# Kernel optimization log

Hardware: AMD Instinct MI355X
Metric: run time of the kernel (lower is better)

The kernel has to match this reference:

```python
import jax, jax.numpy as jnp
import numpy as np

# EventPropLinear constants (match init_kwargs)
DT = 1.0
TAU_M = 10.0
TAU_S = 1.0
AM = 1.0 - DT / TAU_M   # membrane decay
BM = DT / TAU_M         # membrane input coupling
AS = 1.0 - DT / TAU_S   # synaptic decay


def setup_inputs() -> dict:
    key = jax.random.key(0)
    k1, k2 = jax.random.split(key)
    T, B, IN, OUT = 128, 64, 1024, 1024
    x = jax.random.uniform(k1, (T, B, IN), dtype=jnp.float32)  # input drive / spikes in [0,1)
    # torch.nn.init.normal_(weight, mu, mu) with mu=0.1 -> mean 0.1, std 0.1
    weight = 0.1 + 0.1 * jax.random.normal(k2, (OUT, IN), dtype=jnp.float32)
    return {"x": x, "weight": weight}


def _forward_core(x, weight):
    # x: [T, B, IN]; weight: [OUT, IN]
    T, B, _ = x.shape
    O = weight.shape[0]
    # step i (1..T-1) uses input[i-1]; precompute the linear drive once
    cur = jnp.einsum('tbi,oi->tbo', x[:-1], weight)  # [T-1, B, OUT]

    def step(carry, c):
        V, I = carry
        Vn = AM * V + BM * I
        In = AS * I + c
        s = (Vn > 1.0).astype(x.dtype)
        Vn = (1.0 - s) * Vn           # reset on spike
        return (Vn, In), (s, In)

    z = jnp.zeros((B, O), x.dtype)
    _, (spk, Iseq) = jax.lax.scan(step, (z, z), cur)
    zrow = jnp.zeros((1, B, O), x.dtype)
    out = jnp.concatenate([zrow, spk], axis=0)      # output[0] = 0
    I_full = jnp.concatenate([zrow, Iseq], axis=0)  # I[0] = 0
    return out, I_full


def reference(x, weight):
    # returns spike train [T, B, OUT], matching torch output permuted back to time-major
    return _forward_core(x, weight)[0]
```

## Files before the change

kernel.cpp:

```cpp
#include <hip/hip_runtime.h>
#include <hip/hip_fp8.h>

typedef __attribute__((ext_vector_type(8))) short short8;
typedef __attribute__((ext_vector_type(4))) float f32x4;

__device__ __forceinline__ unsigned short f2bf(float f) {
    unsigned u = __float_as_uint(f);
    u += 0x7FFFu + ((u >> 16) & 1u);
    return (unsigned short)(u >> 16);
}

__device__ __forceinline__ unsigned char f2fp8(float f) {
    __hip_fp8_e4m3 q(f);
    return q.__x;
}

__global__ void eventprop_cvt8_kernel(const float* __restrict__ x, const float* __restrict__ w,
                                      unsigned char* __restrict__ x8, unsigned char* __restrict__ w8,
                                      const int nx, const int ntot)
{
    const int i = blockIdx.x * blockDim.x + threadIdx.x;
    const int e0 = i * 8;
    if (e0 >= ntot) return;
    const float* src;
    unsigned char* dst;
    if (e0 < nx) { src = x + e0; dst = x8 + e0; }
    else         { src = w + (e0 - nx); dst = w8 + (e0 - nx); }
    const float4 f0 = *(const float4*)(src);
    const float4 f1 = *(const float4*)(src + 4);
    uchar4 a, b;
    a.x = f2fp8(f0.x); a.y = f2fp8(f0.y); a.z = f2fp8(f0.z); a.w = f2fp8(f0.w);
    b.x = f2fp8(f1.x); b.y = f2fp8(f1.y); b.z = f2fp8(f1.z); b.w = f2fp8(f1.w);
    uint2 v;
    v.x = *(unsigned int*)&a;
    v.y = *(unsigned int*)&b;
    *(uint2*)dst = v;
}

__global__ __launch_bounds__(256, 4) void eventprop_gemm_fp8_kernel(
    const unsigned char* __restrict__ X8, const unsigned char* __restrict__ W8,
    unsigned short* __restrict__ Cb, const int K, const int N, const int nbn)
{
    __shared__ unsigned char As[128 * 128];
    __shared__ unsigned char Bs[64 * 128];

    const int bid0 = blockIdx.x;
    const int cpx = gridDim.x >> 3;
    const int bid = (bid0 & 7) * cpx + (bid0 >> 3);
    const int bm = bid / nbn, bn = bid % nbn;
    const int m0 = bm * 128, n0 = bn * 64;

    const int tid = threadIdx.x;
    const int lane = tid & 63;
    const int wave = tid >> 6;
    const int wr = wave >> 1, wc = wave & 1;
    const int lrow = lane & 15, kg = lane >> 4;
    const int srow = lane >> 3;
    const int scol = (((lane & 7) ^ srow) * 16);

    f32x4 acc[4][2] = {};

    for (int kt = 0; kt < K; kt += 128) {
        #pragma unroll
        for (int jj = 0; jj < 4; ++jj) {
            const int j = wave * 4 + jj;
            const int row = j * 8 + srow;
            const unsigned char* ga = &X8[(size_t)(m0 + row) * K + kt + scol];
            __builtin_amdgcn_global_load_lds(
                (const __attribute__((address_space(1))) unsigned int*)ga,
                (__attribute__((address_space(3))) unsigned int*)&As[j * 1024], 16, 0, 0);
        }
        #pragma unroll
        for (int jj = 0; jj < 2; ++jj) {
            const int j = wave * 2 + jj;
            const int row = j * 8 + srow;
            const unsigned char* gb = &W8[(size_t)(n0 + row) * K + kt + scol];
            __builtin_amdgcn_global_load_lds(
                (const __attribute__((address_space(1))) unsigned int*)gb,
                (__attribute__((address_space(3))) unsigned int*)&Bs[j * 1024], 16, 0, 0);
        }
        __syncthreads();

        const int rx = (lrow & 7) << 4;
        long a[4][4], b[4][2];
        #pragma unroll
        for (int ks = 0; ks < 4; ++ks) {
            const int cc = (ks * 32 + kg * 8) ^ rx;
            #pragma unroll
            for (int mi = 0; mi < 4; ++mi)
                a[ks][mi] = *(const long*)&As[(wr * 64 + mi * 16 + lrow) * 128 + cc];
            #pragma unroll
            for (int ni = 0; ni < 2; ++ni)
                b[ks][ni] = *(const long*)&Bs[(wc * 32 + ni * 16 + lrow) * 128 + cc];
        }
        #pragma unroll
        for (int ks = 0; ks < 4; ++ks)
            #pragma unroll
            for (int mi = 0; mi < 4; ++mi)
                #pragma unroll
                for (int ni = 0; ni < 2; ++ni)
                    acc[mi][ni] = __builtin_amdgcn_mfma_f32_16x16x32_fp8_fp8(
                        a[ks][mi], b[ks][ni], acc[mi][ni], 0, 0, 0);
        __syncthreads();
    }

    const int r0 = kg * 4;
    #pragma unroll
    for (int mi = 0; mi < 4; ++mi) {
        #pragma unroll
        for (int ni = 0; ni < 2; ++ni) {
            #pragma unroll
            for (int r = 0; r < 4; ++r) {
                const int row = m0 + wr * 64 + mi * 16 + r0 + r;
                const int col = n0 + wc * 32 + ni * 16 + lrow;
                Cb[(size_t)row * N + col] = f2bf(acc[mi][ni][r]);
            }
        }
    }
}

__global__ void eventprop_scan_bf16_kernel(const unsigned short* __restrict__ cur,
                                           float* __restrict__ out, const int BO)
{
    const int j = blockIdx.x * blockDim.x + threadIdx.x;
    const int col = j * 2;
    float V0 = 0.f, I0 = 0.f, V1 = 0.f, I1 = 0.f;
    unsigned int c[8];
    #pragma unroll
    for (int p = 0; p < 8; ++p)
        c[p] = *(const unsigned int*)&cur[(size_t)p * BO + col];
    *(float2*)&out[col] = make_float2(0.f, 0.f);

    #pragma unroll 1
    for (int i = 0; i < 120; i += 8) {
        #pragma unroll
        for (int p = 0; p < 8; ++p) {
            const int it = i + p;
            const unsigned int cn = *(const unsigned int*)&cur[(size_t)(it + 8) * BO + col];
            const float Vn0 = 0.9f * V0 + 0.1f * I0;
            const float Vn1 = 0.9f * V1 + 0.1f * I1;
            const float s0 = (Vn0 > 1.0f) ? 1.0f : 0.0f;
            const float s1 = (Vn1 > 1.0f) ? 1.0f : 0.0f;
            I0 = __uint_as_float(c[p] << 16);
            I1 = __uint_as_float(c[p] & 0xFFFF0000u);
            V0 = (1.0f - s0) * Vn0;
            V1 = (1.0f - s1) * Vn1;
            *(float2*)&out[(size_t)(it + 1) * BO + col] = make_float2(s0, s1);
            c[p] = cn;
        }
    }
    #pragma unroll
    for (int p = 0; p < 7; ++p) {
        const int it = 120 + p;
        const float Vn0 = 0.9f * V0 + 0.1f * I0;
        const float Vn1 = 0.9f * V1 + 0.1f * I1;
        const float s0 = (Vn0 > 1.0f) ? 1.0f : 0.0f;
        const float s1 = (Vn1 > 1.0f) ? 1.0f : 0.0f;
        I0 = __uint_as_float(c[p] << 16);
        I1 = __uint_as_float(c[p] & 0xFFFF0000u);
        V0 = (1.0f - s0) * Vn0;
        V1 = (1.0f - s1) * Vn1;
        *(float2*)&out[(size_t)(it + 1) * BO + col] = make_float2(s0, s1);
    }
}

__global__ __launch_bounds__(256, 2) void eventprop_gemm_f32in_kernel(
    const float* __restrict__ X, const float* __restrict__ W, float* __restrict__ C,
    const int K, const int N, const int nbn)
{
    __shared__ unsigned short As[128][32];
    __shared__ unsigned short Bs[128][32];
    const int bid = blockIdx.x;
    const int bm = bid / nbn, bn = bid % nbn;
    const int m0 = bm * 128, n0 = bn * 128;
    const int tid = threadIdx.x;
    const int lane = tid & 63;
    const int wave = tid >> 6;
    const int wr = wave >> 1, wc = wave & 1;
    const int lrow = lane & 15, kg = lane >> 4;

    f32x4 acc[4][4] = {};
    for (int kt = 0; kt < K; kt += 32) {
        #pragma unroll
        for (int p = 0; p < 4; ++p) {
            const int idx = p * 256 + tid;
            const int row = idx >> 3;
            const int c4  = (idx & 7) * 4;
            const float4 fa = *(const float4*)&X[(size_t)(m0 + row) * K + kt + c4];
            ushort4 ua; ua.x = f2bf(fa.x); ua.y = f2bf(fa.y); ua.z = f2bf(fa.z); ua.w = f2bf(fa.w);
            *(ushort4*)&As[row][c4] = ua;
            const float4 fb = *(const float4*)&W[(size_t)(n0 + row) * K + kt + c4];
            ushort4 ub; ub.x = f2bf(fb.x); ub.y = f2bf(fb.y); ub.z = f2bf(fb.z); ub.w = f2bf(fb.w);
            *(ushort4*)&Bs[row][c4] = ub;
        }
        __syncthreads();
        short8 a[4], b[4];
        #pragma unroll
        for (int mi = 0; mi < 4; ++mi) a[mi] = *(const short8*)&As[wr * 64 + mi * 16 + lrow][kg * 8];
        #pragma unroll
        for (int ni = 0; ni < 4; ++ni) b[ni] = *(const short8*)&Bs[wc * 64 + ni * 16 + lrow][kg * 8];
        #pragma unroll
        for (int mi = 0; mi < 4; ++mi)
            #pragma unroll
            for (int ni = 0; ni < 4; ++ni)
                acc[mi][ni] = __builtin_amdgcn_mfma_f32_16x16x32_bf16(a[mi], b[ni], acc[mi][ni], 0, 0, 0);
        __syncthreads();
    }
    const int r0 = kg * 4;
    #pragma unroll
    for (int mi = 0; mi < 4; ++mi)
        #pragma unroll
        for (int ni = 0; ni < 4; ++ni)
            #pragma unroll
            for (int r = 0; r < 4; ++r)
                C[(size_t)(m0 + wr * 64 + mi * 16 + r0 + r) * N + (n0 + wc * 64 + ni * 16 + lrow)] = acc[mi][ni][r];
}

__global__ void eventprop_scan_kernel(float* __restrict__ out, const int BO)
{
    const int idx = blockIdx.x * blockDim.x + threadIdx.x;
    float V = 0.f, I = 0.f;
    float c[8];
    #pragma unroll
    for (int p = 0; p < 8; ++p)
        c[p] = out[(size_t)p * BO + idx];
    out[idx] = 0.f;
    #pragma unroll 1
    for (int i = 0; i < 120; i += 8) {
        #pragma unroll
        for (int p = 0; p < 8; ++p) {
            const int it = i + p;
            const float cn = out[(size_t)(it + 8) * BO + idx];
            const float Vn = 0.9f * V + 0.1f * I;
            const float s = (Vn > 1.0f) ? 1.0f : 0.0f;
            I = c[p];
            V = (1.0f - s) * Vn;
            out[(size_t)(it + 1) * BO + idx] = s;
            c[p] = cn;
        }
    }
    #pragma unroll
    for (int p = 0; p < 7; ++p) {
        const int it = 120 + p;
        const float Vn = 0.9f * V + 0.1f * I;
        const float s = (Vn > 1.0f) ? 1.0f : 0.0f;
        I = c[p];
        V = (1.0f - s) * Vn;
        out[(size_t)(it + 1) * BO + idx] = s;
    }
}

extern "C" void kernel_launch(void* const* d_in, const int* in_sizes, int n_in,
                              void* d_out, int out_size, void* d_ws, size_t ws_size,
                              hipStream_t stream) {
    const float* x = (const float*)d_in[0];
    const float* w = (const float*)d_in[1];
    float* out = (float*)d_out;

    const int T = 128, B = 64, IN = 1024, OUT = 1024;
    const int Mpad = T * B;
    const int BO = B * OUT;
    const size_t nx = (size_t)Mpad * IN;
    const size_t nw = (size_t)OUT * IN;
    const size_t ncur = (size_t)Mpad * OUT;
    const size_t need = ncur * 2 + nx + nw;

    if (ws_size >= need) {
        unsigned short* curb = (unsigned short*)d_ws;
        unsigned char* x8 = (unsigned char*)(curb + ncur);
        unsigned char* w8 = x8 + nx;
        const int ntot = (int)(nx + nw);
        const int cvt_blocks = (ntot / 8 + 255) / 256;
        eventprop_cvt8_kernel<<<dim3(cvt_blocks), dim3(256), 0, stream>>>(x, w, x8, w8, (int)nx, ntot);
        const int nbn = OUT / 64;
        const int nblocks = (Mpad / 128) * nbn;
        eventprop_gemm_fp8_kernel<<<dim3(nblocks), dim3(256), 0, stream>>>(x8, w8, curb, IN, OUT, nbn);
        eventprop_scan_bf16_kernel<<<dim3((BO / 2) / 256), dim3(256), 0, stream>>>(curb, out, BO);
    } else {
        const int nbn = OUT / 128;
        const int nblocks = (Mpad / 128) * nbn;
        eventprop_gemm_f32in_kernel<<<dim3(nblocks), dim3(256), 0, stream>>>(x, w, out, IN, OUT, nbn);
        eventprop_scan_kernel<<<dim3(BO / 256), dim3(256), 0, stream>>>(out, BO);
    }
}
```

Before: 41.21 us.

## Double-buffer fp8 GEMM LDS tiles with async prefetch two stages ahead

Converts the fp8 GEMM main loop to a double-buffered LDS pipeline: two K-tiles are issued up front, and each iteration waits only on the older tile's loads (vmcnt) before prefetching tile t+2 into the freed buffer while the MFMAs run. The aim is to hide global-to-LDS load latency behind compute instead of serializing load, sync and compute. LDS use doubles to 48KB per block, so launch bounds drop to 3 blocks/CU and occupancy may fall.

```diff
diff --git a/kernel.cpp b/kernel.cpp
--- a/kernel.cpp
+++ b/kernel.cpp
@@ -37,12 +37,12 @@
     *(uint2*)dst = v;
 }
 
-__global__ __launch_bounds__(256, 4) void eventprop_gemm_fp8_kernel(
+__global__ __launch_bounds__(256, 3) void eventprop_gemm_fp8_pipe_kernel(
     const unsigned char* __restrict__ X8, const unsigned char* __restrict__ W8,
     unsigned short* __restrict__ Cb, const int K, const int N, const int nbn)
 {
-    __shared__ unsigned char As[128 * 128];
-    __shared__ unsigned char Bs[64 * 128];
+    __shared__ unsigned char As[2][128 * 128];
+    __shared__ unsigned char Bs[2][64 * 128];
 
     const int bid0 = blockIdx.x;
     const int cpx = gridDim.x >> 3;
@@ -58,9 +58,7 @@
     const int srow = lane >> 3;
     const int scol = (((lane & 7) ^ srow) * 16);
 
-    f32x4 acc[4][2] = {};
-
-    for (int kt = 0; kt < K; kt += 128) {
+    auto stage = [&](int buf, int kt) {
         #pragma unroll
         for (int jj = 0; jj < 4; ++jj) {
             const int j = wave * 4 + jj;
@@ -68,7 +66,7 @@
             const unsigned char* ga = &X8[(size_t)(m0 + row) * K + kt + scol];
             __builtin_amdgcn_global_load_lds(
                 (const __attribute__((address_space(1))) unsigned int*)ga,
-                (__attribute__((address_space(3))) unsigned int*)&As[j * 1024], 16, 0, 0);
+                (__attribute__((address_space(3))) unsigned int*)&As[buf][j * 1024], 16, 0, 0);
         }
         #pragma unroll
         for (int jj = 0; jj < 2; ++jj) {
@@ -77,22 +75,41 @@
             const unsigned char* gb = &W8[(size_t)(n0 + row) * K + kt + scol];
             __builtin_amdgcn_global_load_lds(
                 (const __attribute__((address_space(1))) unsigned int*)gb,
-                (__attribute__((address_space(3))) unsigned int*)&Bs[j * 1024], 16, 0, 0);
-        }
-        __syncthreads();
-
-        const int rx = (lrow & 7) << 4;
+                (__attribute__((address_space(3))) unsigned int*)&Bs[buf][j * 1024], 16, 0, 0);
+        }
+    };
+
+    f32x4 acc[4][2] = {};
+    const int NT = K >> 7;
+    stage(0, 0);
+    stage(1, 128);
+
+    const int rx = (lrow & 7) << 4;
+
+    for (int t = 0; t < NT; ++t) {
+        const int cur = t & 1;
+        if (t + 1 < NT) asm volatile("s_waitcnt vmcnt(6)" ::: "memory");
+        else            asm volatile("s_waitcnt vmcnt(0)" ::: "memory");
+        __builtin_amdgcn_s_barrier();
+        __builtin_amdgcn_sched_barrier(0);
+
         long a[4][4], b[4][2];
         #pragma unroll
         for (int ks = 0; ks < 4; ++ks) {
             const int cc = (ks * 32 + kg * 8) ^ rx;
             #pragma unroll
             for (int mi = 0; mi < 4; ++mi)
-                a[ks][mi] = *(const long*)&As[(wr * 64 + mi * 16 + lrow) * 128 + cc];
+                a[ks][mi] = *(const long*)&As[cur][(wr * 64 + mi * 16 + lrow) * 128 + cc];
             #pragma unroll
             for (int ni = 0; ni < 2; ++ni)
-                b[ks][ni] = *(const long*)&Bs[(wc * 32 + ni * 16 + lrow) * 128 + cc];
-        }
+                b[ks][ni] = *(const long*)&Bs[cur][(wc * 32 + ni * 16 + lrow) * 128 + cc];
+        }
+        asm volatile("s_waitcnt lgkmcnt(0)" ::: "memory");
+        __builtin_amdgcn_sched_barrier(0);
+        __builtin_amdgcn_s_barrier();
+
+        if (t + 2 < NT) stage(cur, (t + 2) << 7);
+
         #pragma unroll
         for (int ks = 0; ks < 4; ++ks)
             #pragma unroll
@@ -101,7 +118,6 @@
                 for (int ni = 0; ni < 2; ++ni)
                     acc[mi][ni] = __builtin_amdgcn_mfma_f32_16x16x32_fp8_fp8(
                         a[ks][mi], b[ks][ni], acc[mi][ni], 0, 0, 0);
-        __syncthreads();
     }
 
     const int r0 = kg * 4;
@@ -274,7 +290,7 @@
         eventprop_cvt8_kernel<<<dim3(cvt_blocks), dim3(256), 0, stream>>>(x, w, x8, w8, (int)nx, ntot);
         const int nbn = OUT / 64;
         const int nblocks = (Mpad / 128) * nbn;
-        eventprop_gemm_fp8_kernel<<<dim3(nblocks), dim3(256), 0, stream>>>(x8, w8, curb, IN, OUT, nbn);
+        eventprop_gemm_fp8_pipe_kernel<<<dim3(nblocks), dim3(256), 0, stream>>>(x8, w8, curb, IN, OUT, nbn);
         eventprop_scan_bf16_kernel<<<dim3((BO / 2) / 256), dim3(256), 0, stream>>>(curb, out, BO);
     } else {
         const int nbn = OUT / 128;
```

Measured after the change: 43.97 us. 6.7% more time.

## Fuse FP8 GEMM with LIF scan by tiling over time per batch row

Applied to the files above, without the earlier changes.

The GEMM is retiled so each block computes all 128 timesteps for one batch index and 64 output columns. The fp32 currents are written to LDS, reusing the A/B staging buffer, and one wave then runs the recurrent scan and writes spikes directly. This removes the bf16 intermediate round-trip through global memory and one kernel launch. In exchange only 64 of 256 threads do the serial scan tail, global A-row reads become strided by batch, and currents stay fp32 instead of being rounded to bf16.

```diff
diff --git a/kernel.cpp b/kernel.cpp
--- a/kernel.cpp
+++ b/kernel.cpp
@@ -37,18 +37,20 @@
     *(uint2*)dst = v;
 }
 
-__global__ __launch_bounds__(256, 4) void eventprop_gemm_fp8_kernel(
+__global__ __launch_bounds__(256, 4) void eventprop_gemm_scan_fp8_kernel(
     const unsigned char* __restrict__ X8, const unsigned char* __restrict__ W8,
-    unsigned short* __restrict__ Cb, const int K, const int N, const int nbn)
-{
-    __shared__ unsigned char As[128 * 128];
-    __shared__ unsigned char Bs[64 * 128];
+    float* __restrict__ out, const int K, const int N, const int nbn)
+{
+    __shared__ float smemf[128 * 65];
+    unsigned char* As = (unsigned char*)smemf;
+    unsigned char* Bs = As + 16384;
+    float* curLds = smemf;
 
     const int bid0 = blockIdx.x;
     const int cpx = gridDim.x >> 3;
     const int bid = (bid0 & 7) * cpx + (bid0 >> 3);
     const int bm = bid / nbn, bn = bid % nbn;
-    const int m0 = bm * 128, n0 = bn * 64;
+    const int n0 = bn * 64;
 
     const int tid = threadIdx.x;
     const int lane = tid & 63;
@@ -64,8 +66,8 @@
         #pragma unroll
         for (int jj = 0; jj < 4; ++jj) {
             const int j = wave * 4 + jj;
-            const int row = j * 8 + srow;
-            const unsigned char* ga = &X8[(size_t)(m0 + row) * K + kt + scol];
+            const int trow = j * 8 + srow;
+            const unsigned char* ga = &X8[(size_t)(trow * 64 + bm) * K + kt + scol];
             __builtin_amdgcn_global_load_lds(
                 (const __attribute__((address_space(1))) unsigned int*)ga,
                 (__attribute__((address_space(3))) unsigned int*)&As[j * 1024], 16, 0, 0);
@@ -111,56 +113,47 @@
         for (int ni = 0; ni < 2; ++ni) {
             #pragma unroll
             for (int r = 0; r < 4; ++r) {
-                const int row = m0 + wr * 64 + mi * 16 + r0 + r;
-                const int col = n0 + wc * 32 + ni * 16 + lrow;
-                Cb[(size_t)row * N + col] = f2bf(acc[mi][ni][r]);
+                const int t = wr * 64 + mi * 16 + r0 + r;
+                const int col = wc * 32 + ni * 16 + lrow;
+                curLds[t * 65 + col] = acc[mi][ni][r];
             }
         }
     }
-}
-
-__global__ void eventprop_scan_bf16_kernel(const unsigned short* __restrict__ cur,
-                                           float* __restrict__ out, const int BO)
-{
-    const int j = blockIdx.x * blockDim.x + threadIdx.x;
-    const int col = j * 2;
-    float V0 = 0.f, I0 = 0.f, V1 = 0.f, I1 = 0.f;
-    unsigned int c[8];
-    #pragma unroll
-    for (int p = 0; p < 8; ++p)
-        c[p] = *(const unsigned int*)&cur[(size_t)p * BO + col];
-    *(float2*)&out[col] = make_float2(0.f, 0.f);
-
-    #pragma unroll 1
-    for (int i = 0; i < 120; i += 8) {
-        #pragma unroll
-        for (int p = 0; p < 8; ++p) {
-            const int it = i + p;
-            const unsigned int cn = *(const unsigned int*)&cur[(size_t)(it + 8) * BO + col];
-            const float Vn0 = 0.9f * V0 + 0.1f * I0;
-            const float Vn1 = 0.9f * V1 + 0.1f * I1;
-            const float s0 = (Vn0 > 1.0f) ? 1.0f : 0.0f;
-            const float s1 = (Vn1 > 1.0f) ? 1.0f : 0.0f;
-            I0 = __uint_as_float(c[p] << 16);
-            I1 = __uint_as_float(c[p] & 0xFFFF0000u);
-            V0 = (1.0f - s0) * Vn0;
-            V1 = (1.0f - s1) * Vn1;
-            *(float2*)&out[(size_t)(it + 1) * BO + col] = make_float2(s0, s1);
-            c[p] = cn;
-        }
-    }
-    #pragma unroll
-    for (int p = 0; p < 7; ++p) {
-        const int it = 120 + p;
-        const float Vn0 = 0.9f * V0 + 0.1f * I0;
-        const float Vn1 = 0.9f * V1 + 0.1f * I1;
-        const float s0 = (Vn0 > 1.0f) ? 1.0f : 0.0f;
-        const float s1 = (Vn1 > 1.0f) ? 1.0f : 0.0f;
-        I0 = __uint_as_float(c[p] << 16);
-        I1 = __uint_as_float(c[p] & 0xFFFF0000u);
-        V0 = (1.0f - s0) * Vn0;
-        V1 = (1.0f - s1) * Vn1;
-        *(float2*)&out[(size_t)(it + 1) * BO + col] = make_float2(s0, s1);
+    __syncthreads();
+
+    if (tid < 64) {
+        const int col = tid;
+        const size_t obase = (size_t)bm * N + n0 + col;
+        const int BO = 64 * N;
+        float V = 0.f, I = 0.f;
+        float c[8];
+        #pragma unroll
+        for (int p = 0; p < 8; ++p)
+            c[p] = curLds[p * 65 + col];
+        out[obase] = 0.f;
+        #pragma unroll 1
+        for (int i = 0; i < 120; i += 8) {
+            #pragma unroll
+            for (int p = 0; p < 8; ++p) {
+                const int it = i + p;
+                const float cn = curLds[(it + 8) * 65 + col];
+                const float Vn = 0.9f * V + 0.1f * I;
+                const float s = (Vn > 1.0f) ? 1.0f : 0.0f;
+                I = c[p];
+                V = (1.0f - s) * Vn;
+                out[(size_t)(it + 1) * BO + obase] = s;
+                c[p] = cn;
+            }
+        }
+        #pragma unroll
+        for (int p = 0; p < 7; ++p) {
+            const int it = 120 + p;
+            const float Vn = 0.9f * V + 0.1f * I;
+            const float s = (Vn > 1.0f) ? 1.0f : 0.0f;
+            I = c[p];
+            V = (1.0f - s) * Vn;
+            out[(size_t)(it + 1) * BO + obase] = s;
+        }
     }
 }
 
@@ -262,20 +255,17 @@
     const int BO = B * OUT;
     const size_t nx = (size_t)Mpad * IN;
     const size_t nw = (size_t)OUT * IN;
-    const size_t ncur = (size_t)Mpad * OUT;
-    const size_t need = ncur * 2 + nx + nw;
+    const size_t need = nx + nw;
 
     if (ws_size >= need) {
-        unsigned short* curb = (unsigned short*)d_ws;
-        unsigned char* x8 = (unsigned char*)(curb + ncur);
+        unsigned char* x8 = (unsigned char*)d_ws;
         unsigned char* w8 = x8 + nx;
         const int ntot = (int)(nx + nw);
         const int cvt_blocks = (ntot / 8 + 255) / 256;
         eventprop_cvt8_kernel<<<dim3(cvt_blocks), dim3(256), 0, stream>>>(x, w, x8, w8, (int)nx, ntot);
         const int nbn = OUT / 64;
-        const int nblocks = (Mpad / 128) * nbn;
-        eventprop_gemm_fp8_kernel<<<dim3(nblocks), dim3(256), 0, stream>>>(x8, w8, curb, IN, OUT, nbn);
-        eventprop_scan_bf16_kernel<<<dim3((BO / 2) / 256), dim3(256), 0, stream>>>(curb, out, BO);
+        const int nblocks = B * nbn;
+        eventprop_gemm_scan_fp8_kernel<<<dim3(nblocks), dim3(256), 0, stream>>>(x8, w8, out, IN, OUT, nbn);
     } else {
         const int nbn = OUT / 128;
         const int nblocks = (Mpad / 128) * nbn;
```

Measured after the change: 34.70 us, median of 2. 1.19x faster.
